# Optimization experiments

Measured on AMD Instinct MI355X. Metric: run time of the kernel, lower is better.

Reference implementation:

```python
import jax, jax.numpy as jnp
import numpy as np

NUM_HEADS = 16

def setup_inputs() -> dict:
    key = jax.random.key(0)
    k1, k2, k3 = jax.random.split(key, 3)
    B, N, C = 2, 2048, 1024
    x = jax.random.normal(k1, (B, N, C), dtype=jnp.float32)
    # Dense layers: qkv (C -> 3C, no bias), proj (C -> C, with bias)
    w_qkv = jax.random.normal(k2, (C, 3 * C), dtype=jnp.float32) * (C ** -0.5)
    w_proj = jax.random.normal(k3, (C, C), dtype=jnp.float32) * (C ** -0.5)
    b_proj = jnp.zeros((C,), dtype=jnp.float32)
    return {"x": x, "w_qkv": w_qkv, "w_proj": w_proj, "b_proj": b_proj}

def reference(x, w_qkv, w_proj, b_proj):
    B, N, C = x.shape
    H = NUM_HEADS
    Dh = C // H
    scale = Dh ** -0.5
    qkv = x @ w_qkv                                   # [B,N,3C]
    qkv = qkv.reshape(B, N, 3, H, Dh)
    qkv = jnp.transpose(qkv, (2, 0, 3, 1, 4))         # [3,B,H,N,Dh]
    q, k, v = qkv[0], qkv[1], qkv[2]
    attn = jnp.einsum('bhnd,bhmd->bhnm', q, k) * scale  # [B,H,N,N]
    attn = jax.nn.softmax(attn, axis=-1)
    out = jnp.einsum('bhnm,bhmd->bhnd', attn, v)        # [B,H,N,Dh]
    out = jnp.transpose(out, (0, 2, 1, 3)).reshape(B, N, C)
    return out @ w_proj + b_proj
```

## Files before the change

### kernel.cpp

```cpp
#include <hip/hip_runtime.h>
#include <stdint.h>


typedef unsigned short u16;
typedef uint32_t u32;
typedef __bf16 bf16x8 __attribute__((ext_vector_type(8)));
typedef unsigned short u16x8 __attribute__((ext_vector_type(8)));
typedef float f32x4 __attribute__((ext_vector_type(4)));
typedef float f32x16 __attribute__((ext_vector_type(16)));
typedef uint32_t u32x4v __attribute__((ext_vector_type(4)));

#define DEV static __device__ __forceinline__

DEV u16 f2bf(float f) {
    uint32_t u = __float_as_uint(f);
    u += 0x7fffu + ((u >> 16) & 1u);
    return (u16)(u >> 16);
}

DEV u32 cvtpk(float lo, float hi_) {
    u32 r;
    asm("v_cvt_pk_bf16_f32 %0, %1, %2" : "=v"(r) : "v"(lo), "v"(hi_));
    return r;
}
DEV void plswap(u32& x, u32& y) {
    asm("v_permlane32_swap_b32 %0, %1" : "+v"(x), "+v"(y));
}
DEV float exp2f_fast(float x) {
    float r;
    asm("v_exp_f32 %0, %1" : "=v"(r) : "v"(x));
    return r;
}

DEV void gload_lds16(const void* g, void* l) {
    __builtin_amdgcn_global_load_lds(
        (const __attribute__((address_space(1))) uint32_t*)g,
        (__attribute__((address_space(3))) uint32_t*)l, 16, 0, 0);
}

DEV bf16x8 swz_load16(const u16* base, int row, int kbyte) {
    int off = (row * 128 + kbyte) ^ ((row & 7) << 4);
    return *reinterpret_cast<const bf16x8*>(reinterpret_cast<const char*>(base) + off);
}


__global__ void cvt_x_kernel(const float* __restrict__ in, u16* __restrict__ out) {
    int t = blockIdx.x * 256 + threadIdx.x;
    const float4* p = reinterpret_cast<const float4*>(in) + (size_t)t * 2;
    float4 a = p[0], b = p[1];
    u16x8 o;
    o[0] = f2bf(a.x); o[1] = f2bf(a.y); o[2] = f2bf(a.z); o[3] = f2bf(a.w);
    o[4] = f2bf(b.x); o[5] = f2bf(b.y); o[6] = f2bf(b.z); o[7] = f2bf(b.w);
    reinterpret_cast<u16x8*>(out)[t] = o;
}

__global__ void trw_kernel(const float* __restrict__ in, u16* __restrict__ out, int R, int Cc) {
    __shared__ float T[32][33];
    int x = blockIdx.x * 32 + threadIdx.x;
    int y0 = blockIdx.y * 32;
#pragma unroll
    for (int i = 0; i < 4; i++) {
        int y = y0 + threadIdx.y + i * 8;
        T[threadIdx.y + i * 8][threadIdx.x] = in[(size_t)y * Cc + x];
    }
    __syncthreads();
    int xo = y0 + threadIdx.x;
    int yo0 = blockIdx.x * 32;
#pragma unroll
    for (int i = 0; i < 4; i++) {
        int yo = yo0 + threadIdx.y + i * 8;
        out[(size_t)yo * R + xo] = f2bf(T[threadIdx.x][threadIdx.y + i * 8]);
    }
}

__global__ void trv_kernel(const u16* __restrict__ v, u16* __restrict__ vt) {
    __shared__ u16 T[64][72];
    int bh = blockIdx.y, t = blockIdx.x, tid = threadIdx.x;
    const u16* vb = v + (size_t)bh * 2048 * 64;
    u16* vo = vt + (size_t)bh * 64 * 2048;
#pragma unroll
    for (int i = 0; i < 2; i++) {
        int c = tid + i * 256, row = c >> 3, c8 = c & 7;
        u16x8 a = *reinterpret_cast<const u16x8*>(vb + (size_t)(t * 64 + row) * 64 + c8 * 8);
#pragma unroll
        for (int j = 0; j < 8; j++) T[row][c8 * 8 + j] = a[j];
    }
    __syncthreads();
#pragma unroll
    for (int i = 0; i < 2; i++) {
        int c = tid + i * 256, drow = c >> 3, c8 = c & 7;
        u16x8 o;
#pragma unroll
        for (int j = 0; j < 8; j++) o[j] = T[c8 * 8 + j][drow];
        *reinterpret_cast<u16x8*>(vo + (size_t)drow * 2048 + t * 64 + c8 * 8) = o;
    }
}


template <int EPI>
__global__ __launch_bounds__(256, 2) void gemm_kernel(
    const u16* __restrict__ A, const u16* __restrict__ Bt, int ntiles,
    u16* __restrict__ o_q, u16* __restrict__ o_k, u16* __restrict__ o_v,
    float* __restrict__ o_f, const float* __restrict__ bias) {
    __shared__ __align__(16) u16 Al[128 * 64];
    __shared__ __align__(16) u16 Bl[128 * 64];
    int tid = threadIdx.x;
    int bm = blockIdx.x / ntiles, bn = blockIdx.x % ntiles;
    int lane = tid & 63, w = tid >> 6;
    int wr = w >> 1, wc = w & 1;
    int l15 = lane & 15, lhi = lane >> 4;

    f32x4 acc[4][4];
#pragma unroll
    for (int i = 0; i < 4; i++)
#pragma unroll
        for (int j = 0; j < 4; j++) acc[i][j] = (f32x4){0.f, 0.f, 0.f, 0.f};

    for (int kt = 0; kt < 16; ++kt) {
#pragma unroll
        for (int i = 0; i < 4; i++) {
            int lin = w * 4096 + i * 1024 + lane * 16;
            int row = lin >> 7;
            int src = (lin & 127) ^ ((row & 7) << 4);
            gload_lds16((const char*)A + (size_t)(bm * 128 + row) * 2048 + (size_t)kt * 128 + src,
                        (char*)Al + lin);
            gload_lds16((const char*)Bt + (size_t)(bn * 128 + row) * 2048 + (size_t)kt * 128 + src,
                        (char*)Bl + lin);
        }
        __syncthreads();
#pragma unroll
        for (int ks = 0; ks < 2; ++ks) {
            bf16x8 af[4], bfr[4];
#pragma unroll
            for (int mi = 0; mi < 4; ++mi) af[mi] = swz_load16(Al, wr * 64 + mi * 16 + l15, ks * 64 + lhi * 16);
#pragma unroll
            for (int ni = 0; ni < 4; ++ni) bfr[ni] = swz_load16(Bl, wc * 64 + ni * 16 + l15, ks * 64 + lhi * 16);
            __builtin_amdgcn_s_setprio(1);
#pragma unroll
            for (int mi = 0; mi < 4; ++mi)
#pragma unroll
                for (int ni = 0; ni < 4; ++ni)
                    acc[mi][ni] = __builtin_amdgcn_mfma_f32_16x16x32_bf16(af[mi], bfr[ni], acc[mi][ni], 0, 0, 0);
            __builtin_amdgcn_s_setprio(0);
        }
        __syncthreads();
    }

    int row0 = bm * 128 + wr * 64, col0 = bn * 128 + wc * 64;
    if (EPI == 0) {
#pragma unroll
        for (int mi = 0; mi < 4; mi++)
#pragma unroll
            for (int ni = 0; ni < 4; ni++) {
                int col = col0 + ni * 16 + l15;
                int sel = col >> 10, cc = col & 1023;
                int h = cc >> 6, d = cc & 63;
#pragma unroll
                for (int j = 0; j < 4; j++) {
                    int r = row0 + mi * 16 + lhi * 4 + j;
                    int b = r >> 11, n = r & 2047;
                    size_t idx = (((size_t)(b * 16 + h)) * 2048 + n) * 64 + d;
                    float v = acc[mi][ni][j];
                    if (sel == 0) o_q[idx] = f2bf(v * 0.18033688f);
                    else if (sel == 1) o_k[idx] = f2bf(v);
                    else o_v[idx] = f2bf(v);
                }
            }
    } else {
#pragma unroll
        for (int mi = 0; mi < 4; mi++)
#pragma unroll
            for (int ni = 0; ni < 4; ni++) {
                int col = col0 + ni * 16 + l15;
                float bb = bias[col];
#pragma unroll
                for (int j = 0; j < 4; j++) {
                    int r = row0 + mi * 16 + lhi * 4 + j;
                    o_f[(size_t)r * 1024 + col] = acc[mi][ni][j] + bb;
                }
            }
    }
}

__global__ __launch_bounds__(512, 4) void flash6_kernel(
    const u16* __restrict__ qg, const u16* __restrict__ kg, const u16* __restrict__ vtg,
    u16* __restrict__ o) {
    __shared__ __align__(16) char smem[65536];

    int tid = threadIdx.x, lane = tid & 63, w = tid >> 6;
    int wg = w & 3, g = w >> 2;
    int l31 = lane & 31, hi = lane >> 5;
    int p = blockIdx.y * 16 + blockIdx.x;
    int bh = p & 31, qt = p >> 5;
    int q0 = qt * 128 + wg * 32;

#define KL(gg, bb) (smem + ((gg) * 2 + (bb)) * 8192)
#define VL(gg, bb) (smem + 32768 + ((gg) * 2 + (bb)) * 8192)

    const u16* qp = qg + ((size_t)bh * 2048 + q0 + l31) * 64 + hi * 8;
    bf16x8 qf[4];
#pragma unroll
    for (int ds = 0; ds < 4; ds++) qf[ds] = *reinterpret_cast<const bf16x8*>(qp + ds * 16);

    const char* kbg = (const char*)(kg + (size_t)bh * 2048 * 64) + (size_t)g * 16 * 8192;
    const char* vbg = (const char*)(vtg + (size_t)bh * 64 * 2048) + (size_t)g * 2048;

    int srow = lane >> 1, sinner = (lane & 1) * 16;
    int fbase = l31 * 32 + hi * 16;

#define STAGE(bb, tt)                                                                     \
    {                                                                                     \
        _Pragma("unroll") for (int i = 0; i < 2; i++) {                                   \
            gload_lds16(kbg + (size_t)(tt) * 8192 + (i * 32 + srow) * 128 + wg * 32 + sinner, \
                        KL(g, bb) + wg * 2048 + i * 1024 + lane * 16);                    \
            gload_lds16(vbg + (size_t)(i * 32 + srow) * 4096 + (size_t)(tt) * 128 + wg * 32 + sinner, \
                        VL(g, bb) + wg * 2048 + i * 1024 + lane * 16);                    \
        }                                                                                 \
    }

    f32x16 accO[2];
#pragma unroll
    for (int db = 0; db < 2; db++)
#pragma unroll
        for (int r = 0; r < 16; r++) accO[db][r] = 0.f;
    float lsum = 0.f;

    STAGE(0, 0);
    __syncthreads();

    for (int pp = 0; pp < 16; ++pp) {
        int c = pp & 1;
        if (pp < 15) STAGE(c ^ 1, pp + 1);

        bf16x8 ka[2][4];
#pragma unroll
        for (int kvb = 0; kvb < 2; kvb++)
#pragma unroll
            for (int ds = 0; ds < 4; ds++)
                ka[kvb][ds] = *reinterpret_cast<const bf16x8*>(KL(g, c) + ds * 2048 + kvb * 1024 + fbase);
        f32x16 s[2];
        __builtin_amdgcn_s_setprio(1);
#pragma unroll
        for (int kvb = 0; kvb < 2; kvb++) {
#pragma unroll
            for (int r = 0; r < 16; r++) s[kvb][r] = 0.f;
#pragma unroll
            for (int ds = 0; ds < 4; ds++)
                s[kvb] = __builtin_amdgcn_mfma_f32_32x32x16_bf16(ka[kvb][ds], qf[ds], s[kvb], 0, 0, 0);
        }
        __builtin_amdgcn_s_setprio(0);

#pragma unroll
        for (int kvb = 0; kvb < 2; kvb++)
#pragma unroll
            for (int r = 0; r < 16; r++) s[kvb][r] = exp2f_fast(s[kvb][r]);
        float t_[8];
#pragma unroll
        for (int r = 0; r < 8; r++)
            t_[r] = (s[0][r] + s[0][r + 8]) + (s[1][r] + s[1][r + 8]);
#pragma unroll
        for (int r = 0; r < 4; r++) t_[r] += t_[r + 4];
        float rs = (t_[0] + t_[1]) + (t_[2] + t_[3]);
        rs += __shfl_xor(rs, 32);
        lsum += rs;

        bf16x8 pb[4];
#pragma unroll
        for (int kvb = 0; kvb < 2; kvb++) {
            u32 x0 = cvtpk(s[kvb][0], s[kvb][1]), y0 = cvtpk(s[kvb][4], s[kvb][5]);
            u32 x1 = cvtpk(s[kvb][2], s[kvb][3]), y1 = cvtpk(s[kvb][6], s[kvb][7]);
            u32 x2 = cvtpk(s[kvb][8], s[kvb][9]), y2 = cvtpk(s[kvb][12], s[kvb][13]);
            u32 x3 = cvtpk(s[kvb][10], s[kvb][11]), y3 = cvtpk(s[kvb][14], s[kvb][15]);
            plswap(x0, y0); plswap(x1, y1); plswap(x2, y2); plswap(x3, y3);
            u32x4v plo = {x0, x1, y0, y1};
            u32x4v phi = {x2, x3, y2, y3};
            pb[2 * kvb] = __builtin_bit_cast(bf16x8, plo);
            pb[2 * kvb + 1] = __builtin_bit_cast(bf16x8, phi);
        }

        bf16x8 va[2][4];
#pragma unroll
        for (int db = 0; db < 2; db++)
#pragma unroll
            for (int ks = 0; ks < 4; ks++)
                va[db][ks] = *reinterpret_cast<const bf16x8*>(VL(g, c) + ks * 2048 + db * 1024 + fbase);
        __builtin_amdgcn_s_setprio(1);
#pragma unroll
        for (int db = 0; db < 2; db++)
#pragma unroll
            for (int ks = 0; ks < 4; ks++)
                accO[db] = __builtin_amdgcn_mfma_f32_32x32x16_bf16(va[db][ks], pb[ks], accO[db], 0, 0, 0);
        __builtin_amdgcn_s_setprio(0);

        __syncthreads();
    }
#undef STAGE

    float* mbuf = (float*)smem;
    int base = (wg * 64 + lane) * 36;
    if (g == 1) {
#pragma unroll
        for (int db = 0; db < 2; db++)
#pragma unroll
            for (int q4 = 0; q4 < 4; q4++) {
                f32x4 v4 = {accO[db][q4 * 4 + 0], accO[db][q4 * 4 + 1],
                            accO[db][q4 * 4 + 2], accO[db][q4 * 4 + 3]};
                *reinterpret_cast<f32x4*>(mbuf + base + db * 16 + q4 * 4) = v4;
            }
        mbuf[base + 32] = lsum;
    }
    __syncthreads();
    if (g == 0) {
        float lsum2 = mbuf[base + 32];
        float inv = 1.f / (lsum + lsum2);
        int b = bh >> 4, h = bh & 15;
        u16* ob = o + ((size_t)(b * 2048 + q0 + l31)) * 1024 + h * 64;
#pragma unroll
        for (int db = 0; db < 2; db++) {
            f32x4 m4[4];
#pragma unroll
            for (int q4 = 0; q4 < 4; q4++)
                m4[q4] = *reinterpret_cast<const f32x4*>(mbuf + base + db * 16 + q4 * 4);
#pragma unroll
            for (int i = 0; i < 8; i++) {
                int r = 2 * i;
                int d = (r & 3) + 8 * (r >> 2) + 4 * hi + 32 * db;
                float lo = (accO[db][r] + m4[r >> 2][r & 3]) * inv;
                float hi_ = (accO[db][r + 1] + m4[(r + 1) >> 2][(r + 1) & 3]) * inv;
                *reinterpret_cast<u32*>(ob + d) = cvtpk(lo, hi_);
            }
        }
    }
#undef KL
#undef VL
}


extern "C" void kernel_launch(void* const* d_in, const int* in_sizes, int n_in,
                              void* d_out, int out_size, void* d_ws, size_t ws_size,
                              hipStream_t stream) {
    (void)in_sizes; (void)n_in; (void)out_size; (void)ws_size;
    const float* x = (const float*)d_in[0];
    const float* w_qkv = (const float*)d_in[1];
    const float* w_proj = (const float*)d_in[2];
    const float* b_proj = (const float*)d_in[3];
    float* out = (float*)d_out;
    char* ws = (char*)d_ws;

    u16* xb   = (u16*)(ws + 0);
    u16* wqt  = (u16*)(ws + 8388608);
    u16* wpt  = (u16*)(ws + 14680064);
    u16* qws  = (u16*)(ws + 16777216);
    u16* kws  = (u16*)(ws + 25165824);
    u16* vws  = (u16*)(ws + 33554432);
    u16* vtws = (u16*)(ws + 41943040);
    u16* attn = (u16*)(ws + 50331648);

    cvt_x_kernel<<<2048, 256, 0, stream>>>(x, xb);
    trw_kernel<<<dim3(96, 32), dim3(32, 8), 0, stream>>>(w_qkv, wqt, 1024, 3072);
    trw_kernel<<<dim3(32, 32), dim3(32, 8), 0, stream>>>(w_proj, wpt, 1024, 1024);
    gemm_kernel<0><<<32 * 24, 256, 0, stream>>>(xb, wqt, 24, qws, kws, vws, nullptr, nullptr);
    trv_kernel<<<dim3(32, 32), 256, 0, stream>>>(vws, vtws);
    flash6_kernel<<<dim3(16, 32), 512, 0, stream>>>(qws, kws, vtws, attn);
    gemm_kernel<1><<<32 * 8, 256, 0, stream>>>(attn, wpt, 8, nullptr, nullptr, nullptr, out, b_proj);
}
```

Baseline: 113.3 us.

## Double-buffer GEMM LDS tiles, fuse prep kernels, hoist row-sum shuffle

The GEMM now double-buffers its A/B LDS tiles, so the global-to-LDS load of the next k-tile is issued before the MFMAs on the current tile, hiding load latency. The three input conversion/transpose kernels are merged into one launch to cut launch overhead. In the attention kernel, the cross-half row-sum shuffle moves out of the loop and runs once at the end. Doubling LDS to 64KB per block may lower occupancy under launch_bounds(256,2).

```diff
diff --git a/kernel.cpp b/kernel.cpp
--- a/kernel.cpp
+++ b/kernel.cpp
@@ -43,33 +43,47 @@
     return *reinterpret_cast<const bf16x8*>(reinterpret_cast<const char*>(base) + off);
 }
 
-
-__global__ void cvt_x_kernel(const float* __restrict__ in, u16* __restrict__ out) {
-    int t = blockIdx.x * 256 + threadIdx.x;
-    const float4* p = reinterpret_cast<const float4*>(in) + (size_t)t * 2;
-    float4 a = p[0], b = p[1];
-    u16x8 o;
-    o[0] = f2bf(a.x); o[1] = f2bf(a.y); o[2] = f2bf(a.z); o[3] = f2bf(a.w);
-    o[4] = f2bf(b.x); o[5] = f2bf(b.y); o[6] = f2bf(b.z); o[7] = f2bf(b.w);
-    reinterpret_cast<u16x8*>(out)[t] = o;
-}
-
-__global__ void trw_kernel(const float* __restrict__ in, u16* __restrict__ out, int R, int Cc) {
+__global__ __launch_bounds__(256) void prep_kernel(
+    const float* __restrict__ x, u16* __restrict__ xb,
+    const float* __restrict__ wq, u16* __restrict__ wqt,
+    const float* __restrict__ wp, u16* __restrict__ wpt) {
     __shared__ float T[32][33];
-    int x = blockIdx.x * 32 + threadIdx.x;
-    int y0 = blockIdx.y * 32;
+    int b = blockIdx.x, tid = threadIdx.x;
+    if (b < 2048) {
+        int t = b * 256 + tid;
+        const float4* p = reinterpret_cast<const float4*>(x) + (size_t)t * 2;
+        float4 a = p[0], c = p[1];
+        u16x8 o;
+        o[0] = f2bf(a.x); o[1] = f2bf(a.y); o[2] = f2bf(a.z); o[3] = f2bf(a.w);
+        o[4] = f2bf(c.x); o[5] = f2bf(c.y); o[6] = f2bf(c.z); o[7] = f2bf(c.w);
+        reinterpret_cast<u16x8*>(xb)[t] = o;
+        return;
+    }
+    const float* in;
+    u16* out;
+    int bx, by, R = 1024, Cc;
+    if (b < 5120) {
+        int idx = b - 2048;
+        bx = idx % 96; by = idx / 96; Cc = 3072; in = wq; out = wqt;
+    } else {
+        int idx = b - 5120;
+        bx = idx % 32; by = idx / 32; Cc = 1024; in = wp; out = wpt;
+    }
+    int tx = tid & 31, ty = tid >> 5;
+    int xcol = bx * 32 + tx;
+    int y0 = by * 32;
 #pragma unroll
     for (int i = 0; i < 4; i++) {
-        int y = y0 + threadIdx.y + i * 8;
-        T[threadIdx.y + i * 8][threadIdx.x] = in[(size_t)y * Cc + x];
-    }
-    __syncthreads();
-    int xo = y0 + threadIdx.x;
-    int yo0 = blockIdx.x * 32;
+        int y = y0 + ty + i * 8;
+        T[ty + i * 8][tx] = in[(size_t)y * Cc + xcol];
+    }
+    __syncthreads();
+    int xo = y0 + tx;
+    int yo0 = bx * 32;
 #pragma unroll
     for (int i = 0; i < 4; i++) {
-        int yo = yo0 + threadIdx.y + i * 8;
-        out[(size_t)yo * R + xo] = f2bf(T[threadIdx.x][threadIdx.y + i * 8]);
+        int yo = yo0 + ty + i * 8;
+        out[(size_t)yo * R + xo] = f2bf(T[tx][ty + i * 8]);
     }
 }
 
@@ -102,8 +116,8 @@
     const u16* __restrict__ A, const u16* __restrict__ Bt, int ntiles,
     u16* __restrict__ o_q, u16* __restrict__ o_k, u16* __restrict__ o_v,
     float* __restrict__ o_f, const float* __restrict__ bias) {
-    __shared__ __align__(16) u16 Al[128 * 64];
-    __shared__ __align__(16) u16 Bl[128 * 64];
+    __shared__ __align__(16) u16 Al[2][8192];
+    __shared__ __align__(16) u16 Bl[2][8192];
     int tid = threadIdx.x;
     int bm = blockIdx.x / ntiles, bn = blockIdx.x % ntiles;
     int lane = tid & 63, w = tid >> 6;
@@ -116,25 +130,32 @@
 #pragma unroll
         for (int j = 0; j < 4; j++) acc[i][j] = (f32x4){0.f, 0.f, 0.f, 0.f};
 
+#define GSTAGE(bb, kt_)                                                                       \
+    {                                                                                         \
+        _Pragma("unroll") for (int i = 0; i < 4; i++) {                                       \
+            int lin = w * 4096 + i * 1024 + lane * 16;                                        \
+            int row = lin >> 7;                                                               \
+            int src = (lin & 127) ^ ((row & 7) << 4);                                         \
+            gload_lds16((const char*)A + (size_t)(bm * 128 + row) * 2048 + (size_t)(kt_)*128 + src, \
+                        (char*)Al[bb] + lin);                                                 \
+            gload_lds16((const char*)Bt + (size_t)(bn * 128 + row) * 2048 + (size_t)(kt_)*128 + src, \
+                        (char*)Bl[bb] + lin);                                                 \
+        }                                                                                     \
+    }
+
+    GSTAGE(0, 0);
+    __syncthreads();
+
     for (int kt = 0; kt < 16; ++kt) {
-#pragma unroll
-        for (int i = 0; i < 4; i++) {
-            int lin = w * 4096 + i * 1024 + lane * 16;
-            int row = lin >> 7;
-            int src = (lin & 127) ^ ((row & 7) << 4);
-            gload_lds16((const char*)A + (size_t)(bm * 128 + row) * 2048 + (size_t)kt * 128 + src,
-                        (char*)Al + lin);
-            gload_lds16((const char*)Bt + (size_t)(bn * 128 + row) * 2048 + (size_t)kt * 128 + src,
-                        (char*)Bl + lin);
-        }
-        __syncthreads();
+        int cur = kt & 1;
+        if (kt < 15) GSTAGE(cur ^ 1, kt + 1);
 #pragma unroll
         for (int ks = 0; ks < 2; ++ks) {
             bf16x8 af[4], bfr[4];
 #pragma unroll
-            for (int mi = 0; mi < 4; ++mi) af[mi] = swz_load16(Al, wr * 64 + mi * 16 + l15, ks * 64 + lhi * 16);
-#pragma unroll
-            for (int ni = 0; ni < 4; ++ni) bfr[ni] = swz_load16(Bl, wc * 64 + ni * 16 + l15, ks * 64 + lhi * 16);
+            for (int mi = 0; mi < 4; ++mi) af[mi] = swz_load16(Al[cur], wr * 64 + mi * 16 + l15, ks * 64 + lhi * 16);
+#pragma unroll
+            for (int ni = 0; ni < 4; ++ni) bfr[ni] = swz_load16(Bl[cur], wc * 64 + ni * 16 + l15, ks * 64 + lhi * 16);
             __builtin_amdgcn_s_setprio(1);
 #pragma unroll
             for (int mi = 0; mi < 4; ++mi)
@@ -145,6 +166,7 @@
         }
         __syncthreads();
     }
+#undef GSTAGE
 
     int row0 = bm * 128 + wr * 64, col0 = bn * 128 + wc * 64;
     if (EPI == 0) {
@@ -260,9 +282,7 @@
             t_[r] = (s[0][r] + s[0][r + 8]) + (s[1][r] + s[1][r + 8]);
 #pragma unroll
         for (int r = 0; r < 4; r++) t_[r] += t_[r + 4];
-        float rs = (t_[0] + t_[1]) + (t_[2] + t_[3]);
-        rs += __shfl_xor(rs, 32);
-        lsum += rs;
+        lsum += (t_[0] + t_[1]) + (t_[2] + t_[3]);
 
         bf16x8 pb[4];
 #pragma unroll
@@ -296,6 +316,8 @@
     }
 #undef STAGE
 
+    lsum += __shfl_xor(lsum, 32);
+
     float* mbuf = (float*)smem;
     int base = (wg * 64 + lane) * 36;
     if (g == 1) {
@@ -356,9 +378,7 @@
     u16* vtws = (u16*)(ws + 41943040);
     u16* attn = (u16*)(ws + 50331648);
 
-    cvt_x_kernel<<<2048, 256, 0, stream>>>(x, xb);
-    trw_kernel<<<dim3(96, 32), dim3(32, 8), 0, stream>>>(w_qkv, wqt, 1024, 3072);
-    trw_kernel<<<dim3(32, 32), dim3(32, 8), 0, stream>>>(w_proj, wpt, 1024, 1024);
+    prep_kernel<<<6144, 256, 0, stream>>>(x, xb, w_qkv, wqt, w_proj, wpt);
     gemm_kernel<0><<<32 * 24, 256, 0, stream>>>(xb, wqt, 24, qws, kws, vws, nullptr, nullptr);
     trv_kernel<<<dim3(32, 32), 256, 0, stream>>>(vws, vtws);
     flash6_kernel<<<dim3(16, 32), 512, 0, stream>>>(qws, kws, vtws, attn);
```

Measured after the change: 117.4 us. 1.04x slower.
